# Optimization experiments

Hardware: AMD Instinct MI355X
Metric: run time of the kernel (lower is better)

Reference implementation:

```python
import jax, jax.numpy as jnp
import numpy as np

EPS = 1e-12
B, S, H, NH, L, F = 8, 512, 768, 12, 12, 3072
V, TV, P = 21128, 2, 512
DH = H // NH


def layer_norm(x, g, b):
    m = jnp.mean(x, axis=-1, keepdims=True)
    v = jnp.var(x, axis=-1, keepdims=True)
    return g * (x - m) / jnp.sqrt(v + EPS) + b


def setup_inputs() -> dict:
    key = jax.random.key(0)
    ks = iter(jax.random.split(key, 40))
    r = lambda shape: (jax.random.normal(next(ks), shape, jnp.float32) * 0.02)
    inp = {
        "input_ids": jax.random.randint(next(ks), (B, S), 0, V, jnp.int32),
        "segment_ids": jax.random.randint(next(ks), (B, S), 0, TV, jnp.int32),
        "attention_mask": jnp.ones((B, 1, 1, S), jnp.float32),
        "tok_emb": r((V, H)),
        "pos_emb": r((P, H)),
        "type_emb": r((TV, H)),
        "emb_g": jnp.ones((H,), jnp.float32),
        "emb_b": jnp.zeros((H,), jnp.float32),
        # stacked per-layer params [L, ...]
        "Wq": r((L, H, H)), "bq": jnp.zeros((L, H), jnp.float32),
        "Wk": r((L, H, H)), "bk": jnp.zeros((L, H), jnp.float32),
        "Wv": r((L, H, H)), "bv": jnp.zeros((L, H), jnp.float32),
        "Wao": r((L, H, H)), "bao": jnp.zeros((L, H), jnp.float32),
        "ln1_g": jnp.ones((L, H), jnp.float32), "ln1_b": jnp.zeros((L, H), jnp.float32),
        "Wi": r((L, H, F)), "bi": jnp.zeros((L, F), jnp.float32),
        "Wio": r((L, F, H)), "bio": jnp.zeros((L, H), jnp.float32),
        "ln2_g": jnp.ones((L, H), jnp.float32), "ln2_b": jnp.zeros((L, H), jnp.float32),
    }
    return inp


def reference(input_ids, segment_ids, attention_mask,
              tok_emb, pos_emb, type_emb, emb_g, emb_b,
              Wq, bq, Wk, bk, Wv, bv, Wao, bao, ln1_g, ln1_b,
              Wi, bi, Wio, bio, ln2_g, ln2_b):
    # ---- embedding: token + type + position, then LayerNorm ----
    x = tok_emb[input_ids] + type_emb[segment_ids] + pos_emb[None, :S, :]
    x = layer_norm(x, emb_g, emb_b)  # [B,S,H]

    mask_add = (1.0 - attention_mask) * -10000.0  # [B,1,1,S]
    scale = 1.0 / jnp.sqrt(jnp.asarray(DH, x.dtype))

    def split_heads(t):  # [B,S,H] -> [B,NH,S,DH]
        return t.reshape(B, S, NH, DH).transpose(0, 2, 1, 3)

    for l in range(Wq.shape[0]):
        q = split_heads(x @ Wq[l] + bq[l])
        k = split_heads(x @ Wk[l] + bk[l])
        v = split_heads(x @ Wv[l] + bv[l])
        score = jnp.einsum("bhqd,bhkd->bhqk", q, k) * scale + mask_add
        attn = jax.nn.softmax(score, axis=-1)
        ctx = jnp.einsum("bhqk,bhkd->bhqd", attn, v)
        ctx = ctx.transpose(0, 2, 1, 3).reshape(B, S, H)
        # attention output: dense + residual + LN
        attn_out = layer_norm(ctx @ Wao[l] + bao[l] + x, ln1_g[l], ln1_b[l])
        # FFN: dense-gelu-dense + residual + LN (exact erf gelu as in tf.keras)
        h = jax.nn.gelu(attn_out @ Wi[l] + bi[l], approximate=False)
        x = layer_norm(h @ Wio[l] + bio[l] + attn_out, ln2_g[l], ln2_b[l])

    return x  # sequence output [B,S,H]
```

## Files before the change

kernel.cpp:

```cpp
#include <hip/hip_runtime.h>
#include <math.h>

static constexpr int Bc = 8;
static constexpr int Sc = 512;
static constexpr int Hc = 768;
static constexpr int NHc = 12;
static constexpr int Lc = 12;
static constexpr int Fc = 3072;
static constexpr int DHc = 64;
static constexpr int NTOK = Bc * Sc;
static constexpr int QKVN = 3 * Hc;

typedef _Float16 h16x8 __attribute__((ext_vector_type(8)));
typedef float f32x4 __attribute__((ext_vector_type(4)));
typedef unsigned short us4 __attribute__((ext_vector_type(4)));
typedef unsigned int u32x4 __attribute__((ext_vector_type(4)));

__device__ __forceinline__ unsigned short f2h(float f) {
    _Float16 h = (_Float16)f;
    return __builtin_bit_cast(unsigned short, h);
}

#define AS1 __attribute__((address_space(1)))
#define AS3 __attribute__((address_space(3)))
__device__ __forceinline__ void gld_lds16(const void* g, void* l) {
    __builtin_amdgcn_global_load_lds((const AS1 void*)g, (AS3 void*)l, 16, 0, 0);
}

__global__ __launch_bounds__(256) void embed_ln_kernel(
    const int* __restrict__ ids, const int* __restrict__ seg,
    const float* __restrict__ tok, const float* __restrict__ typ,
    const float* __restrict__ pos, const float* __restrict__ g,
    const float* __restrict__ b, float* __restrict__ outf,
    unsigned short* __restrict__ outb)
{
    int t = blockIdx.x;
    int si = t % Sc;
    int id = ids[t], sg = seg[t];
    const float* tp = tok + (size_t)id * Hc;
    const float* yp = typ + (size_t)sg * Hc;
    const float* pp = pos + (size_t)si * Hc;

    float e[3];
    float s = 0.f, s2 = 0.f;
#pragma unroll
    for (int j = 0; j < 3; j++) {
        int h = threadIdx.x + j * 256;
        float v = tp[h] + yp[h] + pp[h];
        e[j] = v; s += v; s2 += v * v;
    }
    __shared__ float red[8];
#pragma unroll
    for (int o = 32; o > 0; o >>= 1) { s += __shfl_xor(s, o); s2 += __shfl_xor(s2, o); }
    int lane = threadIdx.x & 63, wid = threadIdx.x >> 6;
    if (lane == 0) { red[wid] = s; red[4 + wid] = s2; }
    __syncthreads();
    if (threadIdx.x == 0) {
        red[0] = red[0] + red[1] + red[2] + red[3];
        red[4] = red[4] + red[5] + red[6] + red[7];
    }
    __syncthreads();
    float mean = red[0] * (1.0f / Hc);
    float var  = red[4] * (1.0f / Hc) - mean * mean;
    float rstd = rsqrtf(var + 1e-12f);
    float* op = outf + (size_t)t * Hc;
    unsigned short* ob = outb + (size_t)t * Hc;
#pragma unroll
    for (int j = 0; j < 3; j++) {
        int h = threadIdx.x + j * 256;
        float v = g[h] * (e[j] - mean) * rstd + b[h];
        op[h] = v;
        ob[h] = f2h(v);
    }
}

__global__ __launch_bounds__(256) void add_ln_kernel(
    const float* __restrict__ tin, const float* __restrict__ res,
    const float* __restrict__ g, const float* __restrict__ b,
    float* __restrict__ outf, unsigned short* __restrict__ outb)
{
    int t = blockIdx.x;
    const float* ip = tin + (size_t)t * Hc;
    const float* rp = res + (size_t)t * Hc;

    float e[3];
    float s = 0.f, s2 = 0.f;
#pragma unroll
    for (int j = 0; j < 3; j++) {
        int h = threadIdx.x + j * 256;
        float v = ip[h] + rp[h];
        e[j] = v; s += v; s2 += v * v;
    }
    __shared__ float red[8];
#pragma unroll
    for (int o = 32; o > 0; o >>= 1) { s += __shfl_xor(s, o); s2 += __shfl_xor(s2, o); }
    int lane = threadIdx.x & 63, wid = threadIdx.x >> 6;
    if (lane == 0) { red[wid] = s; red[4 + wid] = s2; }
    __syncthreads();
    if (threadIdx.x == 0) {
        red[0] = red[0] + red[1] + red[2] + red[3];
        red[4] = red[4] + red[5] + red[6] + red[7];
    }
    __syncthreads();
    float mean = red[0] * (1.0f / Hc);
    float var  = red[4] * (1.0f / Hc) - mean * mean;
    float rstd = rsqrtf(var + 1e-12f);
    float* op = outf + (size_t)t * Hc;
    unsigned short* ob = outb + (size_t)t * Hc;
#pragma unroll
    for (int j = 0; j < 3; j++) {
        int h = threadIdx.x + j * 256;
        float v = g[h] * (e[j] - mean) * rstd + b[h];
        op[h] = v;
        ob[h] = f2h(v);
    }
}

__global__ __launch_bounds__(256) void transpose_conv(
    const float* __restrict__ src, unsigned short* __restrict__ dst,
    int K, int N)
{
    __shared__ float t[32][33];
    int n0 = blockIdx.x * 32, k0 = blockIdx.y * 32;
    int tx = threadIdx.x, ty = threadIdx.y;
#pragma unroll
    for (int j = 0; j < 4; j++)
        t[ty + j * 8][tx] = src[(size_t)(k0 + ty + j * 8) * N + n0 + tx];
    __syncthreads();
#pragma unroll
    for (int j = 0; j < 4; j++)
        dst[(size_t)(n0 + ty + j * 8) * K + k0 + tx] = f2h(t[tx][ty + j * 8]);
}

__global__ void concat3_kernel(const float* __restrict__ a, const float* __restrict__ b,
                               const float* __restrict__ c, float* __restrict__ o)
{
    int i = blockIdx.x * 256 + threadIdx.x;
    float v = (i < 768) ? a[i] : (i < 1536 ? b[i - 768] : c[i - 1536]);
    o[i] = v;
}

template <int OUT>
__global__ __launch_bounds__(256) void gemm_mfma(
    const unsigned short* __restrict__ A,
    const unsigned short* __restrict__ Bt,
    const float* __restrict__ bias,
    float* __restrict__ Cf,
    unsigned short* __restrict__ Cb,
    int M, int N, int K)
{
    __shared__ __align__(16) unsigned short As[128 * 64];
    __shared__ __align__(16) unsigned short Bs[128 * 64];

    int tid = threadIdx.x;
    int l = tid & 63, w = tid >> 6;
    int m0 = blockIdx.x * 128, n0 = blockIdx.y * 128;
    int lr = l & 15;
    int kg = l >> 4;
    int wr = (w >> 1) * 64, wc = (w & 1) * 64;
    int lx = lr & 7;

    f32x4 acc[4][4] = {};

    for (int k0 = 0; k0 < K; k0 += 64) {
#pragma unroll
        for (int p = 0; p < 4; p++) {
            int i = p * 256 + w * 64 + l;
            int row = i >> 3;
            int slot = (i & 7) ^ (row & 7);
            const unsigned short* ga = A + (size_t)(m0 + row) * K + k0 + slot * 8;
            const unsigned short* gb = Bt + (size_t)(n0 + row) * K + k0 + slot * 8;
            unsigned short* la = As + (size_t)(p * 256 + w * 64) * 8;
            unsigned short* lb = Bs + (size_t)(p * 256 + w * 64) * 8;
            gld_lds16(ga, la);
            gld_lds16(gb, lb);
        }
        asm volatile("s_waitcnt vmcnt(0)" ::: "memory");
        __syncthreads();

#pragma unroll
        for (int kh = 0; kh < 2; kh++) {
            h16x8 av[4], bv[4];
#pragma unroll
            for (int f = 0; f < 4; f++) {
                int sl = (kh * 4 + kg) ^ lx;
                av[f] = *(const h16x8*)(As + (wr + f * 16 + lr) * 64 + sl * 8);
                bv[f] = *(const h16x8*)(Bs + (wc + f * 16 + lr) * 64 + sl * 8);
            }
#pragma unroll
            for (int i = 0; i < 4; i++)
#pragma unroll
                for (int j = 0; j < 4; j++)
                    acc[i][j] = __builtin_amdgcn_mfma_f32_16x16x32_f16(
                        av[i], bv[j], acc[i][j], 0, 0, 0);
        }
        __syncthreads();
    }

#pragma unroll
    for (int i = 0; i < 4; i++) {
        int rbase = m0 + wr + i * 16 + kg * 4;
#pragma unroll
        for (int j = 0; j < 4; j++) {
            int col = n0 + wc + j * 16 + lr;
            float bcol = bias[col];
#pragma unroll
            for (int r = 0; r < 4; r++) {
                float v = acc[i][j][r] + bcol;
                if (OUT == 1) {
                    v = 0.5f * v * (1.0f + erff(v * 0.70710678118654752f));
                    Cb[(size_t)(rbase + r) * N + col] = f2h(v);
                } else if (OUT == 2) {
                    Cb[(size_t)(rbase + r) * N + col] = f2h(v);
                } else {
                    Cf[(size_t)(rbase + r) * N + col] = v;
                }
            }
        }
    }
}

__global__ __launch_bounds__(256) void attn_mfma(
    const unsigned short* __restrict__ QKV, const float* __restrict__ mask,
    unsigned short* __restrict__ O)
{
    __shared__ __align__(16) unsigned short Ks[64 * 64];
    __shared__ __align__(16) unsigned short Vt[64 * 64];
    __shared__ float Ml[64];

    int tid = threadIdx.x;
    int l = tid & 63, w = tid >> 6;
    int g = l >> 4, c = l & 15;
    int q0 = blockIdx.x * 64;
    int h = blockIdx.y, bb = blockIdx.z;

    const size_t rowQ = (size_t)(bb * Sc + q0 + w * 16 + c) * QKVN + h * DHc;
    h16x8 qv[2];
    qv[0] = *(const h16x8*)(QKV + rowQ + 8 * g);
    qv[1] = *(const h16x8*)(QKV + rowQ + 32 + 8 * g);

    float m_run = -1e30f, l_run = 0.f;
    f32x4 acc_o[4] = {};
    const float scale = 0.125f;

    for (int kt = 0; kt < Sc; kt += 64) {
        const unsigned short* Kgb = QKV + (size_t)(bb * Sc + kt) * QKVN + Hc + h * DHc;
#pragma unroll
        for (int p = 0; p < 2; p++) {
            int i = p * 256 + tid;
            int row = i >> 3;
            int slot = (i & 7) ^ (row & 7);
            gld_lds16(Kgb + (size_t)row * QKVN + slot * 8, Ks + (size_t)(p * 256 + w * 64) * 8);
        }
        const unsigned short* Vgb = QKV + (size_t)(bb * Sc + kt) * QKVN + 2 * Hc + h * DHc;
        us4 vv[4];
#pragma unroll
        for (int it = 0; it < 4; it++) {
            int kv0 = (w + it * 4) * 4;
#pragma unroll
            for (int j = 0; j < 4; j++)
                vv[it][j] = Vgb[(size_t)(kv0 + j) * QKVN + l];
        }
#pragma unroll
        for (int it = 0; it < 4; it++) {
            int kv0 = (w + it * 4) * 4;
            *(us4*)(Vt + l * 64 + (((kv0 >> 3) ^ (l & 7)) * 8) + (kv0 & 7)) = vv[it];
        }
        if (tid < 64) Ml[tid] = (1.0f - mask[bb * Sc + kt + tid]) * -10000.0f;
        asm volatile("s_waitcnt vmcnt(0)" ::: "memory");
        __syncthreads();

        f32x4 s[4] = {};
#pragma unroll
        for (int kh = 0; kh < 2; kh++) {
#pragma unroll
            for (int f = 0; f < 4; f++) {
                int row = f * 16 + c;
                h16x8 av = *(const h16x8*)(Ks + row * 64 + (((kh * 4 + g) ^ (row & 7)) * 8));
                s[f] = __builtin_amdgcn_mfma_f32_16x16x32_f16(av, qv[kh], s[f], 0, 0, 0);
            }
        }

        f32x4 mv[4];
#pragma unroll
        for (int f = 0; f < 4; f++) mv[f] = *(const f32x4*)&Ml[f * 16 + 4 * g];
        float mx = -1e30f;
#pragma unroll
        for (int f = 0; f < 4; f++)
#pragma unroll
            for (int r = 0; r < 4; r++) {
                float sv = s[f][r] * scale + mv[f][r];
                s[f][r] = sv;
                mx = fmaxf(mx, sv);
            }
        mx = fmaxf(mx, __shfl_xor(mx, 16));
        mx = fmaxf(mx, __shfl_xor(mx, 32));
        float mn = fmaxf(m_run, mx);
        float fs = __expf(m_run - mn);
        m_run = mn;
        float ps = 0.f;
        f32x4 p[4];
#pragma unroll
        for (int f = 0; f < 4; f++)
#pragma unroll
            for (int r = 0; r < 4; r++) {
                float pv = __expf(s[f][r] - mn);
                p[f][r] = pv;
                ps += pv;
            }
        ps += __shfl_xor(ps, 16);
        ps += __shfl_xor(ps, 32);
        l_run = l_run * fs + ps;
#pragma unroll
        for (int fm = 0; fm < 4; fm++)
#pragma unroll
            for (int r = 0; r < 4; r++) acc_o[fm][r] *= fs;

        unsigned pk[4][2];
#pragma unroll
        for (int f = 0; f < 4; f++)
#pragma unroll
            for (int rp = 0; rp < 2; rp++)
                pk[f][rp] = ((unsigned)f2h(p[f][2 * rp + 1]) << 16) | f2h(p[f][2 * rp]);

#pragma unroll
        for (int kh = 0; kh < 2; kh++) {
            u32x4 bw;
#pragma unroll
            for (int t = 0; t < 4; t++) {
                int srcl = (2 * ((l >> 4) & 1) + (t >> 1)) * 16 + c;
                unsigned lo = __shfl(pk[2 * kh][t & 1], srcl);
                unsigned hi = __shfl(pk[2 * kh + 1][t & 1], srcl);
                bw[t] = (g & 2) ? hi : lo;
            }
            h16x8 bfrag = __builtin_bit_cast(h16x8, bw);
#pragma unroll
            for (int fm = 0; fm < 4; fm++) {
                int row = fm * 16 + c;
                h16x8 av = *(const h16x8*)(Vt + row * 64 + (((kh * 4 + g) ^ (row & 7)) * 8));
                acc_o[fm] = __builtin_amdgcn_mfma_f32_16x16x32_f16(av, bfrag, acc_o[fm], 0, 0, 0);
            }
        }
        __syncthreads();
    }

    float rl = 1.0f / l_run;
    size_t tokrow = (size_t)(bb * Sc + q0 + w * 16 + c) * Hc + h * DHc;
#pragma unroll
    for (int fm = 0; fm < 4; fm++) {
        us4 ob;
#pragma unroll
        for (int r = 0; r < 4; r++) ob[r] = f2h(acc_o[fm][r] * rl);
        *(us4*)(O + tokrow + fm * 16 + 4 * g) = ob;
    }
}

extern "C" void kernel_launch(void* const* d_in, const int* in_sizes, int n_in,
                              void* d_out, int out_size, void* d_ws, size_t ws_size,
                              hipStream_t stream)
{
    const int*   input_ids      = (const int*)  d_in[0];
    const int*   segment_ids    = (const int*)  d_in[1];
    const float* attention_mask = (const float*)d_in[2];
    const float* tok_emb = (const float*)d_in[3];
    const float* pos_emb = (const float*)d_in[4];
    const float* type_emb= (const float*)d_in[5];
    const float* emb_g   = (const float*)d_in[6];
    const float* emb_b   = (const float*)d_in[7];
    const float* Wq  = (const float*)d_in[8];  const float* bq  = (const float*)d_in[9];
    const float* Wk  = (const float*)d_in[10]; const float* bk  = (const float*)d_in[11];
    const float* Wv  = (const float*)d_in[12]; const float* bv  = (const float*)d_in[13];
    const float* Wao = (const float*)d_in[14]; const float* bao = (const float*)d_in[15];
    const float* ln1_g = (const float*)d_in[16]; const float* ln1_b = (const float*)d_in[17];
    const float* Wi  = (const float*)d_in[18]; const float* bi  = (const float*)d_in[19];
    const float* Wio = (const float*)d_in[20]; const float* bio = (const float*)d_in[21];
    const float* ln2_g = (const float*)d_in[22]; const float* ln2_b = (const float*)d_in[23];

    float* out = (float*)d_out;

    const size_t NT = (size_t)NTOK * Hc;
    float* Xf  = (float*)d_ws;
    float* XAf = Xf + NT;
    float* Tf  = XAf + NT;
    unsigned short* QKVb = (unsigned short*)(Tf + NT);
    unsigned short* Xb  = QKVb + (size_t)NTOK * QKVN;
    unsigned short* XAb = Xb + NT;
    unsigned short* Cb  = XAb + NT;
    unsigned short* Hb  = Cb + NT;
    unsigned short* WqkvT = Hb + (size_t)NTOK * Fc;
    unsigned short* WaoT  = WqkvT + (size_t)QKVN * Hc;
    unsigned short* WiT   = WaoT + (size_t)Hc * Hc;
    unsigned short* WioT  = WiT + (size_t)Fc * Hc;
    float* bqkv = (float*)(WioT + (size_t)Hc * Fc);

    embed_ln_kernel<<<NTOK, 256, 0, stream>>>(input_ids, segment_ids, tok_emb,
                                              type_emb, pos_emb, emb_g, emb_b, Xf, Xb);

    dim3 tb(32, 8);
    dim3 gQKV(NTOK / 128, QKVN / 128);
    dim3 gH(NTOK / 128, Hc / 128);
    dim3 gF(NTOK / 128, Fc / 128);
    dim3 gA(Sc / 64, NHc, Bc);

    for (int l = 0; l < Lc; l++) {
        const float* wq  = Wq  + (size_t)l * Hc * Hc;
        const float* wk  = Wk  + (size_t)l * Hc * Hc;
        const float* wv  = Wv  + (size_t)l * Hc * Hc;
        const float* wao = Wao + (size_t)l * Hc * Hc;
        const float* wi  = Wi  + (size_t)l * Hc * Fc;
        const float* wio = Wio + (size_t)l * Fc * Hc;

        transpose_conv<<<dim3(Hc / 32, Hc / 32), tb, 0, stream>>>(wq, WqkvT, Hc, Hc);
        transpose_conv<<<dim3(Hc / 32, Hc / 32), tb, 0, stream>>>(wk, WqkvT + (size_t)Hc * Hc, Hc, Hc);
        transpose_conv<<<dim3(Hc / 32, Hc / 32), tb, 0, stream>>>(wv, WqkvT + (size_t)2 * Hc * Hc, Hc, Hc);
        transpose_conv<<<dim3(Hc / 32, Hc / 32), tb, 0, stream>>>(wao, WaoT, Hc, Hc);
        transpose_conv<<<dim3(Fc / 32, Hc / 32), tb, 0, stream>>>(wi, WiT, Hc, Fc);
        transpose_conv<<<dim3(Hc / 32, Fc / 32), tb, 0, stream>>>(wio, WioT, Fc, Hc);
        concat3_kernel<<<QKVN / 256, 256, 0, stream>>>(bq + (size_t)l * Hc, bk + (size_t)l * Hc,
                                                       bv + (size_t)l * Hc, bqkv);

        gemm_mfma<2><<<gQKV, 256, 0, stream>>>(Xb, WqkvT, bqkv, nullptr, QKVb,
                                               NTOK, QKVN, Hc);
        attn_mfma<<<gA, 256, 0, stream>>>(QKVb, attention_mask, Cb);

        gemm_mfma<0><<<gH, 256, 0, stream>>>(Cb, WaoT, bao + (size_t)l * Hc, Tf, nullptr,
                                             NTOK, Hc, Hc);
        add_ln_kernel<<<NTOK, 256, 0, stream>>>(Tf, Xf, ln1_g + (size_t)l * Hc,
                                                ln1_b + (size_t)l * Hc, XAf, XAb);

        gemm_mfma<1><<<gF, 256, 0, stream>>>(XAb, WiT, bi + (size_t)l * Fc, nullptr, Hb,
                                             NTOK, Fc, Hc);
        gemm_mfma<0><<<gH, 256, 0, stream>>>(Hb, WioT, bio + (size_t)l * Hc, Tf, nullptr,
                                             NTOK, Hc, Fc);
        float* xout = (l == Lc - 1) ? out : Xf;
        add_ln_kernel<<<NTOK, 256, 0, stream>>>(Tf, XAf, ln2_g + (size_t)l * Hc,
                                                ln2_b + (size_t)l * Hc, xout, Xb);
    }
}
```

Before: 2.359 ms.

## Batch weight prep into one kernel, emit V transposed, store GEMM outputs in fp16

All per-layer weight transposes and fp16 conversions, plus the QKV bias concatenation, move into a single prep kernel launched once for all layers. This removes 84 small launches. The QKV GEMM now writes V directly in a transposed [B,NH,DH,S] layout, so attention can load V tiles with async global-to-LDS copies instead of strided scalar gathers. The dense-output GEMMs store fp16 instead of fp32 before add+LayerNorm, which halves that traffic but reduces precision of the pre-LN sum.

```diff
diff --git a/kernel.cpp b/kernel.cpp
--- a/kernel.cpp
+++ b/kernel.cpp
@@ -11,6 +11,12 @@
 static constexpr int NTOK = Bc * Sc;
 static constexpr int QKVN = 3 * Hc;
 
+static constexpr size_t W_QKV_OFF = 0;
+static constexpr size_t W_AO_OFF  = 1769472;
+static constexpr size_t W_I_OFF   = 2359296;
+static constexpr size_t W_IO_OFF  = 4718592;
+static constexpr size_t LW        = 7077888;
+
 typedef _Float16 h16x8 __attribute__((ext_vector_type(8)));
 typedef float f32x4 __attribute__((ext_vector_type(4)));
 typedef unsigned short us4 __attribute__((ext_vector_type(4)));
@@ -25,6 +31,56 @@
 #define AS3 __attribute__((address_space(3)))
 __device__ __forceinline__ void gld_lds16(const void* g, void* l) {
     __builtin_amdgcn_global_load_lds((const AS1 void*)g, (AS3 void*)l, 16, 0, 0);
+}
+
+__global__ __launch_bounds__(256) void prep_kernel(
+    const float* __restrict__ Wq, const float* __restrict__ Wk,
+    const float* __restrict__ Wv, const float* __restrict__ Wao,
+    const float* __restrict__ Wi, const float* __restrict__ Wio,
+    const float* __restrict__ bq, const float* __restrict__ bk,
+    const float* __restrict__ bv, unsigned short* __restrict__ WALL,
+    float* __restrict__ BALL)
+{
+    int t = blockIdx.x, l = blockIdx.y;
+    int tid = threadIdx.x;
+
+    if (t >= 6912) {
+        int idx = (t - 6912) * 256 + tid;
+        float v = (idx < 768) ? bq[l * Hc + idx]
+                : (idx < 1536) ? bk[l * Hc + idx - 768]
+                               : bv[l * Hc + idx - 1536];
+        BALL[(size_t)l * QKVN + idx] = v;
+        return;
+    }
+
+    const float* src;
+    unsigned short* dst;
+    int K, N, ntn, local;
+    if (t < 2304) {
+        int mat = t / 576; local = t % 576;
+        K = 768; N = 768; ntn = 24;
+        src = (mat == 0 ? Wq : mat == 1 ? Wk : mat == 2 ? Wv : Wao) + (size_t)l * 589824;
+        dst = WALL + (size_t)l * LW + (mat < 3 ? (size_t)mat * 589824 : W_AO_OFF);
+    } else if (t < 4608) {
+        local = t - 2304; K = 768; N = 3072; ntn = 96;
+        src = Wi + (size_t)l * 2359296;
+        dst = WALL + (size_t)l * LW + W_I_OFF;
+    } else {
+        local = t - 4608; K = 3072; N = 768; ntn = 24;
+        src = Wio + (size_t)l * 2359296;
+        dst = WALL + (size_t)l * LW + W_IO_OFF;
+    }
+    int n0 = (local % ntn) * 32, k0 = (local / ntn) * 32;
+    int tx = tid & 31, ty = tid >> 5;
+
+    __shared__ float tl[32][33];
+#pragma unroll
+    for (int j = 0; j < 4; j++)
+        tl[ty + j * 8][tx] = src[(size_t)(k0 + ty + j * 8) * N + n0 + tx];
+    __syncthreads();
+#pragma unroll
+    for (int j = 0; j < 4; j++)
+        dst[(size_t)(n0 + ty + j * 8) * K + k0 + tx] = f2h(tl[tx][ty + j * 8]);
 }
 
 __global__ __launch_bounds__(256) void embed_ln_kernel(
@@ -75,12 +131,12 @@
 }
 
 __global__ __launch_bounds__(256) void add_ln_kernel(
-    const float* __restrict__ tin, const float* __restrict__ res,
+    const unsigned short* __restrict__ tin, const float* __restrict__ res,
     const float* __restrict__ g, const float* __restrict__ b,
     float* __restrict__ outf, unsigned short* __restrict__ outb)
 {
     int t = blockIdx.x;
-    const float* ip = tin + (size_t)t * Hc;
+    const unsigned short* ip = tin + (size_t)t * Hc;
     const float* rp = res + (size_t)t * Hc;
 
     float e[3];
@@ -88,7 +144,7 @@
 #pragma unroll
     for (int j = 0; j < 3; j++) {
         int h = threadIdx.x + j * 256;
-        float v = ip[h] + rp[h];
+        float v = (float)__builtin_bit_cast(_Float16, ip[h]) + rp[h];
         e[j] = v; s += v; s2 += v * v;
     }
     __shared__ float red[8];
@@ -116,37 +172,13 @@
     }
 }
 
-__global__ __launch_bounds__(256) void transpose_conv(
-    const float* __restrict__ src, unsigned short* __restrict__ dst,
-    int K, int N)
-{
-    __shared__ float t[32][33];
-    int n0 = blockIdx.x * 32, k0 = blockIdx.y * 32;
-    int tx = threadIdx.x, ty = threadIdx.y;
-#pragma unroll
-    for (int j = 0; j < 4; j++)
-        t[ty + j * 8][tx] = src[(size_t)(k0 + ty + j * 8) * N + n0 + tx];
-    __syncthreads();
-#pragma unroll
-    for (int j = 0; j < 4; j++)
-        dst[(size_t)(n0 + ty + j * 8) * K + k0 + tx] = f2h(t[tx][ty + j * 8]);
-}
-
-__global__ void concat3_kernel(const float* __restrict__ a, const float* __restrict__ b,
-                               const float* __restrict__ c, float* __restrict__ o)
-{
-    int i = blockIdx.x * 256 + threadIdx.x;
-    float v = (i < 768) ? a[i] : (i < 1536 ? b[i - 768] : c[i - 1536]);
-    o[i] = v;
-}
-
 template <int OUT>
 __global__ __launch_bounds__(256) void gemm_mfma(
     const unsigned short* __restrict__ A,
     const unsigned short* __restrict__ Bt,
     const float* __restrict__ bias,
-    float* __restrict__ Cf,
     unsigned short* __restrict__ Cb,
+    unsigned short* __restrict__ VTp,
     int M, int N, int K)
 {
     __shared__ __align__(16) unsigned short As[128 * 64];
@@ -204,16 +236,21 @@
         for (int j = 0; j < 4; j++) {
             int col = n0 + wc + j * 16 + lr;
             float bcol = bias[col];
-#pragma unroll
-            for (int r = 0; r < 4; r++) {
-                float v = acc[i][j][r] + bcol;
-                if (OUT == 1) {
-                    v = 0.5f * v * (1.0f + erff(v * 0.70710678118654752f));
-                    Cb[(size_t)(rbase + r) * N + col] = f2h(v);
-                } else if (OUT == 2) {
-                    Cb[(size_t)(rbase + r) * N + col] = f2h(v);
-                } else {
-                    Cf[(size_t)(rbase + r) * N + col] = v;
+            if (OUT == 3 && col >= 1536) {
+                int vcol = col - 1536;
+                int hh = vcol >> 6, d = vcol & 63;
+                int bbb = rbase >> 9, s0 = rbase & 511;
+                us4 ob;
+#pragma unroll
+                for (int r = 0; r < 4; r++) ob[r] = f2h(acc[i][j][r] + bcol);
+                *(us4*)(VTp + ((((size_t)bbb * NHc + hh) * DHc + d) << 9) + s0) = ob;
+            } else {
+                int ldc = (OUT == 3) ? 1536 : N;
+#pragma unroll
+                for (int r = 0; r < 4; r++) {
+                    float v = acc[i][j][r] + bcol;
+                    if (OUT == 1) v = 0.5f * v * (1.0f + erff(v * 0.70710678118654752f));
+                    Cb[(size_t)(rbase + r) * ldc + col] = f2h(v);
                 }
             }
         }
@@ -221,9 +258,10 @@
 }
 
 __global__ __launch_bounds__(256) void attn_mfma(
-    const unsigned short* __restrict__ QKV, const float* __restrict__ mask,
-    unsigned short* __restrict__ O)
-{
+    const unsigned short* __restrict__ QK, const unsigned short* __restrict__ VT,
+    const float* __restrict__ mask, unsigned short* __restrict__ O)
+{
+    const int LD = 1536;
     __shared__ __align__(16) unsigned short Ks[64 * 64];
     __shared__ __align__(16) unsigned short Vt[64 * 64];
     __shared__ float Ml[64];
@@ -234,37 +272,31 @@
     int q0 = blockIdx.x * 64;
     int h = blockIdx.y, bb = blockIdx.z;
 
-    const size_t rowQ = (size_t)(bb * Sc + q0 + w * 16 + c) * QKVN + h * DHc;
+    const size_t rowQ = (size_t)(bb * Sc + q0 + w * 16 + c) * LD + h * DHc;
     h16x8 qv[2];
-    qv[0] = *(const h16x8*)(QKV + rowQ + 8 * g);
-    qv[1] = *(const h16x8*)(QKV + rowQ + 32 + 8 * g);
+    qv[0] = *(const h16x8*)(QK + rowQ + 8 * g);
+    qv[1] = *(const h16x8*)(QK + rowQ + 32 + 8 * g);
 
     float m_run = -1e30f, l_run = 0.f;
     f32x4 acc_o[4] = {};
     const float scale = 0.125f;
 
     for (int kt = 0; kt < Sc; kt += 64) {
-        const unsigned short* Kgb = QKV + (size_t)(bb * Sc + kt) * QKVN + Hc + h * DHc;
+        const unsigned short* Kgb = QK + (size_t)(bb * Sc + kt) * LD + Hc + h * DHc;
 #pragma unroll
         for (int p = 0; p < 2; p++) {
             int i = p * 256 + tid;
             int row = i >> 3;
             int slot = (i & 7) ^ (row & 7);
-            gld_lds16(Kgb + (size_t)row * QKVN + slot * 8, Ks + (size_t)(p * 256 + w * 64) * 8);
-        }
-        const unsigned short* Vgb = QKV + (size_t)(bb * Sc + kt) * QKVN + 2 * Hc + h * DHc;
-        us4 vv[4];
-#pragma unroll
-        for (int it = 0; it < 4; it++) {
-            int kv0 = (w + it * 4) * 4;
-#pragma unroll
-            for (int j = 0; j < 4; j++)
-                vv[it][j] = Vgb[(size_t)(kv0 + j) * QKVN + l];
-        }
-#pragma unroll
-        for (int it = 0; it < 4; it++) {
-            int kv0 = (w + it * 4) * 4;
-            *(us4*)(Vt + l * 64 + (((kv0 >> 3) ^ (l & 7)) * 8) + (kv0 & 7)) = vv[it];
+            gld_lds16(Kgb + (size_t)row * LD + slot * 8, Ks + (size_t)(p * 256 + w * 64) * 8);
+        }
+        const unsigned short* Vg = VT + (((size_t)bb * NHc + h) * DHc << 9) + kt;
+#pragma unroll
+        for (int p = 0; p < 2; p++) {
+            int i = p * 256 + tid;
+            int row = i >> 3;
+            int slot = (i & 7) ^ (row & 7);
+            gld_lds16(Vg + ((size_t)row << 9) + slot * 8, Vt + (size_t)(p * 256 + w * 64) * 8);
         }
         if (tid < 64) Ml[tid] = (1.0f - mask[bb * Sc + kt + tid]) * -10000.0f;
         asm volatile("s_waitcnt vmcnt(0)" ::: "memory");
@@ -379,61 +411,51 @@
     float* out = (float*)d_out;
 
     const size_t NT = (size_t)NTOK * Hc;
-    float* Xf  = (float*)d_ws;
-    float* XAf = Xf + NT;
-    float* Tf  = XAf + NT;
-    unsigned short* QKVb = (unsigned short*)(Tf + NT);
-    unsigned short* Xb  = QKVb + (size_t)NTOK * QKVN;
+    float* Xf   = (float*)d_ws;
+    float* XAf  = Xf + NT;
+    float* BALL = XAf + NT;
+    unsigned short* QKb = (unsigned short*)(BALL + (size_t)Lc * QKVN);
+    unsigned short* VT  = QKb + (size_t)NTOK * 1536;
+    unsigned short* Xb  = VT + NT;
     unsigned short* XAb = Xb + NT;
     unsigned short* Cb  = XAb + NT;
-    unsigned short* Hb  = Cb + NT;
-    unsigned short* WqkvT = Hb + (size_t)NTOK * Fc;
-    unsigned short* WaoT  = WqkvT + (size_t)QKVN * Hc;
-    unsigned short* WiT   = WaoT + (size_t)Hc * Hc;
-    unsigned short* WioT  = WiT + (size_t)Fc * Hc;
-    float* bqkv = (float*)(WioT + (size_t)Hc * Fc);
+    unsigned short* Tb  = Cb + NT;
+    unsigned short* Hb  = Tb + NT;
+    unsigned short* WALL = Hb + (size_t)NTOK * Fc;
+
+    prep_kernel<<<dim3(6921, Lc), 256, 0, stream>>>(Wq, Wk, Wv, Wao, Wi, Wio,
+                                                    bq, bk, bv, WALL, BALL);
 
     embed_ln_kernel<<<NTOK, 256, 0, stream>>>(input_ids, segment_ids, tok_emb,
                                               type_emb, pos_emb, emb_g, emb_b, Xf, Xb);
 
-    dim3 tb(32, 8);
     dim3 gQKV(NTOK / 128, QKVN / 128);
     dim3 gH(NTOK / 128, Hc / 128);
     dim3 gF(NTOK / 128, Fc / 128);
     dim3 gA(Sc / 64, NHc, Bc);
 
     for (int l = 0; l < Lc; l++) {
-        const float* wq  = Wq  + (size_t)l * Hc * Hc;
-        const float* wk  = Wk  + (size_t)l * Hc * Hc;
-        const float* wv  = Wv  + (size_t)l * Hc * Hc;
-        const float* wao = Wao + (size_t)l * Hc * Hc;
-        const float* wi  = Wi  + (size_t)l * Hc * Fc;
-        const float* wio = Wio + (size_t)l * Fc * Hc;
-
-        transpose_conv<<<dim3(Hc / 32, Hc / 32), tb, 0, stream>>>(wq, WqkvT, Hc, Hc);
-        transpose_conv<<<dim3(Hc / 32, Hc / 32), tb, 0, stream>>>(wk, WqkvT + (size_t)Hc * Hc, Hc, Hc);
-        transpose_conv<<<dim3(Hc / 32, Hc / 32), tb, 0, stream>>>(wv, WqkvT + (size_t)2 * Hc * Hc, Hc, Hc);
-        transpose_conv<<<dim3(Hc / 32, Hc / 32), tb, 0, stream>>>(wao, WaoT, Hc, Hc);
-        transpose_conv<<<dim3(Fc / 32, Hc / 32), tb, 0, stream>>>(wi, WiT, Hc, Fc);
-        transpose_conv<<<dim3(Hc / 32, Fc / 32), tb, 0, stream>>>(wio, WioT, Fc, Hc);
-        concat3_kernel<<<QKVN / 256, 256, 0, stream>>>(bq + (size_t)l * Hc, bk + (size_t)l * Hc,
-                                                       bv + (size_t)l * Hc, bqkv);
-
-        gemm_mfma<2><<<gQKV, 256, 0, stream>>>(Xb, WqkvT, bqkv, nullptr, QKVb,
+        const unsigned short* WqkvT = WALL + (size_t)l * LW + W_QKV_OFF;
+        const unsigned short* WaoT  = WALL + (size_t)l * LW + W_AO_OFF;
+        const unsigned short* WiT   = WALL + (size_t)l * LW + W_I_OFF;
+        const unsigned short* WioT  = WALL + (size_t)l * LW + W_IO_OFF;
+        const float* bqkv = BALL + (size_t)l * QKVN;
+
+        gemm_mfma<3><<<gQKV, 256, 0, stream>>>(Xb, WqkvT, bqkv, QKb, VT,
                                                NTOK, QKVN, Hc);
-        attn_mfma<<<gA, 256, 0, stream>>>(QKVb, attention_mask, Cb);
-
-        gemm_mfma<0><<<gH, 256, 0, stream>>>(Cb, WaoT, bao + (size_t)l * Hc, Tf, nullptr,
+        attn_mfma<<<gA, 256, 0, stream>>>(QKb, VT, attention_mask, Cb);
+
+        gemm_mfma<2><<<gH, 256, 0, stream>>>(Cb, WaoT, bao + (size_t)l * Hc, Tb, nullptr,
                                              NTOK, Hc, Hc);
-        add_ln_kernel<<<NTOK, 256, 0, stream>>>(Tf, Xf, ln1_g + (size_t)l * Hc,
+        add_ln_kernel<<<NTOK, 256, 0, stream>>>(Tb, Xf, ln1_g + (size_t)l * Hc,
                                                 ln1_b + (size_t)l * Hc, XAf, XAb);
 
-        gemm_mfma<1><<<gF, 256, 0, stream>>>(XAb, WiT, bi + (size_t)l * Fc, nullptr, Hb,
+        gemm_mfma<1><<<gF, 256, 0, stream>>>(XAb, WiT, bi + (size_t)l * Fc, Hb, nullptr,
                                              NTOK, Fc, Hc);
-        gemm_mfma<0><<<gH, 256, 0, stream>>>(Hb, WioT, bio + (size_t)l * Hc, Tf, nullptr,
+        gemm_mfma<2><<<gH, 256, 0, stream>>>(Hb, WioT, bio + (size_t)l * Hc, Tb, nullptr,
                                              NTOK, Hc, Fc);
         float* xout = (l == Lc - 1) ? out : Xf;
-        add_ln_kernel<<<NTOK, 256, 0, stream>>>(Tf, XAf, ln2_g + (size_t)l * Hc,
+        add_ln_kernel<<<NTOK, 256, 0, stream>>>(Tb, XAf, ln2_g + (size_t)l * Hc,
                                                 ln2_b + (size_t)l * Hc, xout, Xb);
     }
 }
```

New measurement: 2.363 ms. No clear change (+0.2%).
